# Optimization experiments

Hardware: AMD Instinct MI355X
Metric: run time of the kernel (lower is better)

## Reference

```python
import jax, jax.numpy as jnp
import numpy as np

D_MODEL = 1024
N_HEADS = 16
D_K = D_MODEL // N_HEADS


def setup_inputs() -> dict:
    key = jax.random.key(0)
    k1, k2, k3 = jax.random.split(key, 3)
    x = jax.random.normal(k1, (2, 2048, D_MODEL), dtype=jnp.float32)
    # torch Linear(d, 3d).weight has shape [3d, d]; y = x @ W.T
    W_qkv = jax.random.normal(k2, (3 * D_MODEL, D_MODEL), dtype=jnp.float32) * (1.0 / np.sqrt(D_MODEL))
    W_out = jax.random.normal(k3, (D_MODEL, D_MODEL), dtype=jnp.float32) * (1.0 / np.sqrt(D_MODEL))
    return {"x": x, "W_qkv": W_qkv, "W_out": W_out}


def reference(x, W_qkv, W_out):
    batch, seq_len, d_model = x.shape
    qkv = jnp.einsum('bsd,ed->bse', x, W_qkv)  # [b, s, 3*d_model]
    qkv = qkv.reshape(batch, seq_len, 3, N_HEADS, D_K)
    qkv = jnp.transpose(qkv, (2, 0, 3, 1, 4))  # [3, b, h, s, dk]
    Q, K, V = qkv[0], qkv[1], qkv[2]
    scale = 1.0 / jnp.sqrt(jnp.asarray(D_K, dtype=x.dtype))
    scores = jnp.einsum('bhqd,bhkd->bhqk', Q, K) * scale  # [b, h, s, s]
    causal = jnp.tril(jnp.ones((seq_len, seq_len), dtype=bool))
    scores = jnp.where(causal, scores, jnp.asarray(-jnp.inf, dtype=scores.dtype))
    attn = jax.nn.softmax(scores, axis=-1)
    out = jnp.einsum('bhqk,bhkd->bhqd', attn, V)  # [b, h, s, dk]
    out = jnp.transpose(out, (0, 2, 1, 3)).reshape(batch, seq_len, d_model)
    return jnp.einsum('bsd,ed->bse', out, W_out)
```

## Files before the change

### kernel.cpp

```cpp
#include <hip/hip_runtime.h>
#include <stdint.h>

#define DMODEL 1024
#define NHEADS 16
#define DKH 64
#define BATCH 2
#define SEQ 2048
#define MTOT (BATCH*SEQ)

typedef __bf16 bf16x8 __attribute__((ext_vector_type(8)));
typedef __bf16 bf16x4 __attribute__((ext_vector_type(4)));
typedef float  f32x4  __attribute__((ext_vector_type(4)));

__device__ __forceinline__ f32x4 mfma16(bf16x8 a, bf16x8 b, f32x4 c){
  return __builtin_amdgcn_mfma_f32_16x16x32_bf16(a, b, c, 0, 0, 0);
}

__device__ __forceinline__ void gload_lds16(const void* g, void* l){
  __builtin_amdgcn_global_load_lds(
      (const __attribute__((address_space(1))) uint32_t*)(uintptr_t)g,
      (__attribute__((address_space(3))) uint32_t*)(uint32_t)(uintptr_t)l,
      16, 0, 0);
}

__device__ __forceinline__ unsigned short f2bf(float f){
  unsigned u = __builtin_bit_cast(unsigned, f);
  u += 0x7fff + ((u >> 16) & 1);
  return (unsigned short)(u >> 16);
}

__global__ void cvt_kernel(const float* __restrict__ in, unsigned short* __restrict__ out, int n4){
  const float4*  in4  = (const float4*)in;
  ushort4*       out4 = (ushort4*)out;
  int i = blockIdx.x * blockDim.x + threadIdx.x;
  int stride = gridDim.x * blockDim.x;
  for (; i < n4; i += stride){
    float4 v = in4[i];
    ushort4 o;
    o.x = f2bf(v.x); o.y = f2bf(v.y); o.z = f2bf(v.z); o.w = f2bf(v.w);
    out4[i] = o;
  }
}

template<int EPI>
__global__ __launch_bounds__(256)
void gemm_bt(const __bf16* __restrict__ Ag, const __bf16* __restrict__ Bg,
             int M, int N, int K,
             __bf16* __restrict__ Qo, __bf16* __restrict__ Ko, __bf16* __restrict__ Vt,
             float* __restrict__ Co){
  __shared__ __align__(16) __bf16 As[128*32];
  __shared__ __align__(16) __bf16 Bs[128*32];
  const int tid  = threadIdx.x;
  const int wave = tid >> 6, lane = tid & 63;
  const int wr = wave >> 1, wc = wave & 1;
  const int lr = lane & 15, lg = lane >> 4;
  const int m0 = blockIdx.y * 128, n0 = blockIdx.x * 128;

  f32x4 acc[4][4] = {};

  const int srow = lane >> 2;
  const int scol = (lane & 3) * 8;
  const __bf16* gA = Ag + (size_t)(m0 + wave*32 + srow) * K + scol;
  const __bf16* gB = Bg + (size_t)(n0 + wave*32 + srow) * K + scol;
  __bf16* lA = &As[(wave*32) * 32];
  __bf16* lB = &Bs[(wave*32) * 32];

  for (int k0 = 0; k0 < K; k0 += 32){
    __syncthreads();
    gload_lds16(gA + k0,                lA);
    gload_lds16(gA + k0 + (size_t)16*K, lA + 16*32);
    gload_lds16(gB + k0,                lB);
    gload_lds16(gB + k0 + (size_t)16*K, lB + 16*32);
    __syncthreads();

    bf16x8 af[4], bfv[4];
#pragma unroll
    for (int i = 0; i < 4; i++)
      af[i] = *(const bf16x8*)&As[(wr*64 + i*16 + lr)*32 + lg*8];
#pragma unroll
    for (int j = 0; j < 4; j++)
      bfv[j] = *(const bf16x8*)&Bs[(wc*64 + j*16 + lr)*32 + lg*8];
#pragma unroll
    for (int i = 0; i < 4; i++)
#pragma unroll
      for (int j = 0; j < 4; j++)
        acc[i][j] = mfma16(af[i], bfv[j], acc[i][j]);
  }

  if (EPI == 0){
    const int three = n0 >> 10;
#pragma unroll
    for (int i = 0; i < 4; i++){
#pragma unroll
      for (int j = 0; j < 4; j++){
#pragma unroll
        for (int r = 0; r < 4; r++){
          int m = m0 + wr*64 + i*16 + lg*4 + r;
          int n = n0 + wc*64 + j*16 + lr;
          int b = m >> 11, s = m & 2047;
          int h = (n >> 6) & 15, dk = n & 63;
          __bf16 val = (__bf16)acc[i][j][r];
          if (three == 0)      Qo[(((size_t)(b*NHEADS + h))*SEQ + s)*DKH + dk] = val;
          else if (three == 1) Ko[(((size_t)(b*NHEADS + h))*SEQ + s)*DKH + dk] = val;
          else                 Vt[(((size_t)(b*NHEADS + h))*DKH + dk)*SEQ + s] = val;
        }
      }
    }
  } else {
#pragma unroll
    for (int i = 0; i < 4; i++)
#pragma unroll
      for (int j = 0; j < 4; j++)
#pragma unroll
        for (int r = 0; r < 4; r++){
          int m = m0 + wr*64 + i*16 + lg*4 + r;
          int n = n0 + wc*64 + j*16 + lr;
          Co[(size_t)m * N + n] = acc[i][j][r];
        }
  }
}

__global__ __launch_bounds__(128)
void attn_kernel(const __bf16* __restrict__ Q, const __bf16* __restrict__ K,
                 const __bf16* __restrict__ Vt, __bf16* __restrict__ Aout){
  const int id   = blockIdx.x;
  const int xcd  = id & 7;
  const int slot = id >> 3;
  const int bh   = (xcd << 2) | (slot >> 5);
  const int j    = slot & 31;
  const int wave = threadIdx.x >> 6, lane = threadIdx.x & 63;
  const int lr = lane & 15, lg = lane >> 4;
  const int swz = (lr & 7) << 4;

  const __bf16* Qh = Q + (size_t)bh*SEQ*DKH;
  const char* Kc = (const char*)(K  + (size_t)bh*SEQ*DKH);
  const char* Vc = (const char*)(Vt + (size_t)bh*DKH*SEQ);

  __shared__ __align__(16) char lds[2][16384];

  const int row8 = lane >> 3;
  const int cG   = ((lane & 7) << 4) ^ (row8 << 4);

  const int b = bh >> 4, h = bh & 15;
  const float k2 = 0.125f * 1.44269504088896340736f;

  for (int ph = 0; ph < 2; ph++){
    const int tb  = ph ? (63 - j) : j;
    const int qw  = tb*32 + wave*16;
    const int nkv = (tb >> 1) + 1;

    bf16x8 qf0 = *(const bf16x8*)(Qh + (size_t)(qw + lr)*DKH + lg*8);
    bf16x8 qf1 = *(const bf16x8*)(Qh + (size_t)(qw + lr)*DKH + 32 + lg*8);

    f32x4 o[4] = {};
    float mrun = -1e30f, lrun = 0.f;

#pragma unroll
    for (int i = 0; i < 4; i++){
      const int srow = wave*32 + i*8 + row8;
      gload_lds16(Kc + (size_t)srow*128 + cG,  &lds[0][wave*4096 + i*1024]);
      gload_lds16(Vc + (size_t)srow*4096 + cG, &lds[0][8192 + wave*4096 + i*1024]);
    }
    __syncthreads();

    for (int kb = 0; kb < nkv; kb++){
      const int kv0 = kb*64;
      if (kb + 1 < nkv){
        const int nv0 = kv0 + 64;
#pragma unroll
        for (int i = 0; i < 4; i++){
          const int srow = wave*32 + i*8 + row8;
          gload_lds16(Kc + (size_t)(nv0 + srow)*128 + cG,
                      &lds[(kb+1)&1][wave*4096 + i*1024]);
          gload_lds16(Vc + (size_t)srow*4096 + (size_t)nv0*2 + cG,
                      &lds[(kb+1)&1][8192 + wave*4096 + i*1024]);
        }
      }
      const char* Ks = lds[kb&1];
      const char* Vs = lds[kb&1] + 8192;

      f32x4 sf[4];
      __builtin_amdgcn_s_setprio(1);
#pragma unroll
      for (int t = 0; t < 4; t++){
        const int row = t*16 + lr;
        bf16x8 kf0 = *(const bf16x8*)(Ks + row*128 + ((lg*16) ^ swz));
        bf16x8 kf1 = *(const bf16x8*)(Ks + row*128 + ((64 + lg*16) ^ swz));
        f32x4 c = {};
        c = mfma16(kf0, qf0, c);
        c = mfma16(kf1, qf1, c);
        sf[t] = c;
      }
      __builtin_amdgcn_s_setprio(0);
      if (kv0 + 63 > qw){
        const int q = qw + lr;
#pragma unroll
        for (int t = 0; t < 4; t++)
#pragma unroll
          for (int r = 0; r < 4; r++){
            int kv = kv0 + t*16 + lg*4 + r;
            sf[t][r] = (kv <= q) ? sf[t][r]*k2 : -1e30f;
          }
      } else {
#pragma unroll
        for (int t = 0; t < 4; t++)
#pragma unroll
          for (int r = 0; r < 4; r++)
            sf[t][r] *= k2;
      }
      float mx = sf[0][0];
#pragma unroll
      for (int t = 0; t < 4; t++)
#pragma unroll
        for (int r = 0; r < 4; r++) mx = fmaxf(mx, sf[t][r]);
      mx = fmaxf(mx, __shfl_xor(mx, 16));
      mx = fmaxf(mx, __shfl_xor(mx, 32));

      float mn = fmaxf(mrun, mx);
      float alpha = __builtin_amdgcn_exp2f(mrun - mn);
      mrun = mn;
      lrun *= alpha;

      float p[16];
#pragma unroll
      for (int t = 0; t < 4; t++)
#pragma unroll
        for (int r = 0; r < 4; r++){
          float v = __builtin_amdgcn_exp2f(sf[t][r] - mn);
          p[t*4 + r] = v;
          lrun += v;
        }

      float av[4];
#pragma unroll
      for (int r = 0; r < 4; r++) av[r] = __shfl(alpha, lg*4 + r);
#pragma unroll
      for (int n = 0; n < 4; n++)
#pragma unroll
        for (int r = 0; r < 4; r++) o[n][r] *= av[r];

      bf16x8 pa0, pa1;
#pragma unroll
      for (int i = 0; i < 8; i++){ pa0[i] = (__bf16)p[i]; pa1[i] = (__bf16)p[8 + i]; }
      __builtin_amdgcn_s_setprio(1);
#pragma unroll
      for (int n = 0; n < 4; n++){
        const int row = n*16 + lr;
        bf16x4 vlo0 = *(const bf16x4*)(Vs + row*128 + ((lg*8) ^ swz));
        bf16x4 vhi0 = *(const bf16x4*)(Vs + row*128 + ((32 + lg*8) ^ swz));
        bf16x4 vlo1 = *(const bf16x4*)(Vs + row*128 + ((64 + lg*8) ^ swz));
        bf16x4 vhi1 = *(const bf16x4*)(Vs + row*128 + ((96 + lg*8) ^ swz));
        bf16x8 vf0 = __builtin_shufflevector(vlo0, vhi0, 0,1,2,3,4,5,6,7);
        bf16x8 vf1 = __builtin_shufflevector(vlo1, vhi1, 0,1,2,3,4,5,6,7);
        o[n] = mfma16(pa0, vf0, o[n]);
        o[n] = mfma16(pa1, vf1, o[n]);
      }
      __builtin_amdgcn_s_setprio(0);
      __syncthreads();
    }

    lrun += __shfl_xor(lrun, 16);
    lrun += __shfl_xor(lrun, 32);
    float inv = 1.0f / lrun;
#pragma unroll
    for (int r = 0; r < 4; r++){
      float invr = __shfl(inv, lg*4 + r);
      __bf16* dst = Aout + ((size_t)b*SEQ + qw + lg*4 + r)*DMODEL + h*DKH;
#pragma unroll
      for (int n = 0; n < 4; n++)
        dst[n*16 + lr] = (__bf16)(o[n][r] * invr);
    }
  }
}

extern "C" void kernel_launch(void* const* d_in, const int* in_sizes, int n_in,
                              void* d_out, int out_size, void* d_ws, size_t ws_size,
                              hipStream_t stream){
  const float* x    = (const float*)d_in[0];
  const float* wqkv = (const float*)d_in[1];
  const float* wout = (const float*)d_in[2];
  float* out = (float*)d_out;
  char* ws = (char*)d_ws;

  __bf16* xb  = (__bf16*)(ws);
  __bf16* Ab  = (__bf16*)(ws);
  __bf16* wqb = (__bf16*)(ws + 8388608);
  __bf16* wob = (__bf16*)(ws + 14680064);
  __bf16* Qb  = (__bf16*)(ws + 16777216);
  __bf16* Kb  = (__bf16*)(ws + 25165824);
  __bf16* Vtb = (__bf16*)(ws + 33554432);

  cvt_kernel<<<1024, 256, 0, stream>>>(x,    (unsigned short*)xb,  (MTOT*DMODEL)/4);
  cvt_kernel<<<1024, 256, 0, stream>>>(wqkv, (unsigned short*)wqb, (3*DMODEL*DMODEL)/4);
  cvt_kernel<<<256,  256, 0, stream>>>(wout, (unsigned short*)wob, (DMODEL*DMODEL)/4);

  gemm_bt<0><<<dim3(24, 32), 256, 0, stream>>>(xb, wqb, MTOT, 3*DMODEL, DMODEL,
                                               Qb, Kb, Vtb, nullptr);
  attn_kernel<<<1024, 128, 0, stream>>>(Qb, Kb, Vtb, Ab);
  gemm_bt<1><<<dim3(8, 32), 256, 0, stream>>>(Ab, wob, MTOT, DMODEL, DMODEL,
                                              nullptr, nullptr, nullptr, out);
}
```

Baseline: 203.5 us.

## Double-buffer GEMM loads, fold softmax scale into Q, lazy rescale in attention

The GEMM now double-buffers its LDS tiles so the next K-slice loads while the current one is multiplied, removing one barrier per iteration. It is templated on tile size, and the output projection uses 128x64 tiles to launch more blocks. The softmax scale times log2(e) is folded into Q in the QKV epilogue, so attention no longer multiplies every score. Attention also skips the running-max rescale unless the new max exceeds the old by more than 8 in log2 units. That lazy rescale is exact after final normalization but allows larger intermediate exponentials, and rounding the pre-scaled Q to bf16 slightly changes numerics.

```diff
diff --git a/kernel.cpp b/kernel.cpp
--- a/kernel.cpp
+++ b/kernel.cpp
@@ -28,6 +28,8 @@
   u += 0x7fff + ((u >> 16) & 1);
   return (unsigned short)(u >> 16);
 }
+
+#define QSCALE 0.1803368801111372f
 
 __global__ void cvt_kernel(const float* __restrict__ in, unsigned short* __restrict__ out, int n4){
   const float4*  in4  = (const float4*)in;
@@ -42,79 +44,93 @@
   }
 }
 
-template<int EPI>
+template<int EPI, int BM, int BN>
 __global__ __launch_bounds__(256)
 void gemm_bt(const __bf16* __restrict__ Ag, const __bf16* __restrict__ Bg,
              int M, int N, int K,
              __bf16* __restrict__ Qo, __bf16* __restrict__ Ko, __bf16* __restrict__ Vt,
              float* __restrict__ Co){
-  __shared__ __align__(16) __bf16 As[128*32];
-  __shared__ __align__(16) __bf16 Bs[128*32];
+  constexpr int AM = BM/32;
+  constexpr int AN = BN/32;
+  constexpr int CA = BM/64;
+  constexpr int CB = BN/64;
+  __shared__ __align__(16) __bf16 As[2][BM*32];
+  __shared__ __align__(16) __bf16 Bs[2][BN*32];
   const int tid  = threadIdx.x;
   const int wave = tid >> 6, lane = tid & 63;
   const int wr = wave >> 1, wc = wave & 1;
   const int lr = lane & 15, lg = lane >> 4;
-  const int m0 = blockIdx.y * 128, n0 = blockIdx.x * 128;
-
-  f32x4 acc[4][4] = {};
+  const int m0 = blockIdx.y * BM, n0 = blockIdx.x * BN;
+
+  f32x4 acc[AM][AN] = {};
 
   const int srow = lane >> 2;
   const int scol = (lane & 3) * 8;
-  const __bf16* gA = Ag + (size_t)(m0 + wave*32 + srow) * K + scol;
-  const __bf16* gB = Bg + (size_t)(n0 + wave*32 + srow) * K + scol;
-  __bf16* lA = &As[(wave*32) * 32];
-  __bf16* lB = &Bs[(wave*32) * 32];
-
-  for (int k0 = 0; k0 < K; k0 += 32){
+  const __bf16* gA = Ag + (size_t)(m0 + wave*(BM/4) + srow) * K + scol;
+  const __bf16* gB = Bg + (size_t)(n0 + wave*(BN/4) + srow) * K + scol;
+
+  const int nk = K >> 5;
+
+#pragma unroll
+  for (int c = 0; c < CA; c++)
+    gload_lds16(gA + (size_t)(c*16)*K, &As[0][(wave*(BM/4) + c*16)*32]);
+#pragma unroll
+  for (int c = 0; c < CB; c++)
+    gload_lds16(gB + (size_t)(c*16)*K, &Bs[0][(wave*(BN/4) + c*16)*32]);
+
+  for (int t = 0; t < nk; t++){
     __syncthreads();
-    gload_lds16(gA + k0,                lA);
-    gload_lds16(gA + k0 + (size_t)16*K, lA + 16*32);
-    gload_lds16(gB + k0,                lB);
-    gload_lds16(gB + k0 + (size_t)16*K, lB + 16*32);
-    __syncthreads();
-
-    bf16x8 af[4], bfv[4];
-#pragma unroll
-    for (int i = 0; i < 4; i++)
-      af[i] = *(const bf16x8*)&As[(wr*64 + i*16 + lr)*32 + lg*8];
-#pragma unroll
-    for (int j = 0; j < 4; j++)
-      bfv[j] = *(const bf16x8*)&Bs[(wc*64 + j*16 + lr)*32 + lg*8];
-#pragma unroll
-    for (int i = 0; i < 4; i++)
-#pragma unroll
-      for (int j = 0; j < 4; j++)
+    if (t + 1 < nk){
+      const int k0 = (t+1) << 5, b = (t+1) & 1;
+#pragma unroll
+      for (int c = 0; c < CA; c++)
+        gload_lds16(gA + k0 + (size_t)(c*16)*K, &As[b][(wave*(BM/4) + c*16)*32]);
+#pragma unroll
+      for (int c = 0; c < CB; c++)
+        gload_lds16(gB + k0 + (size_t)(c*16)*K, &Bs[b][(wave*(BN/4) + c*16)*32]);
+    }
+    const int cb = t & 1;
+    bf16x8 af[AM], bfv[AN];
+#pragma unroll
+    for (int i = 0; i < AM; i++)
+      af[i] = *(const bf16x8*)&As[cb][(wr*(BM/2) + i*16 + lr)*32 + lg*8];
+#pragma unroll
+    for (int j = 0; j < AN; j++)
+      bfv[j] = *(const bf16x8*)&Bs[cb][(wc*(BN/2) + j*16 + lr)*32 + lg*8];
+#pragma unroll
+    for (int i = 0; i < AM; i++)
+#pragma unroll
+      for (int j = 0; j < AN; j++)
         acc[i][j] = mfma16(af[i], bfv[j], acc[i][j]);
   }
 
   if (EPI == 0){
     const int three = n0 >> 10;
 #pragma unroll
-    for (int i = 0; i < 4; i++){
-#pragma unroll
-      for (int j = 0; j < 4; j++){
+    for (int i = 0; i < AM; i++){
+#pragma unroll
+      for (int j = 0; j < AN; j++){
 #pragma unroll
         for (int r = 0; r < 4; r++){
-          int m = m0 + wr*64 + i*16 + lg*4 + r;
-          int n = n0 + wc*64 + j*16 + lr;
+          int m = m0 + wr*(BM/2) + i*16 + lg*4 + r;
+          int n = n0 + wc*(BN/2) + j*16 + lr;
           int b = m >> 11, s = m & 2047;
           int h = (n >> 6) & 15, dk = n & 63;
-          __bf16 val = (__bf16)acc[i][j][r];
-          if (three == 0)      Qo[(((size_t)(b*NHEADS + h))*SEQ + s)*DKH + dk] = val;
-          else if (three == 1) Ko[(((size_t)(b*NHEADS + h))*SEQ + s)*DKH + dk] = val;
-          else                 Vt[(((size_t)(b*NHEADS + h))*DKH + dk)*SEQ + s] = val;
+          if (three == 0)      Qo[(((size_t)(b*NHEADS + h))*SEQ + s)*DKH + dk] = (__bf16)(acc[i][j][r] * QSCALE);
+          else if (three == 1) Ko[(((size_t)(b*NHEADS + h))*SEQ + s)*DKH + dk] = (__bf16)acc[i][j][r];
+          else                 Vt[(((size_t)(b*NHEADS + h))*DKH + dk)*SEQ + s] = (__bf16)acc[i][j][r];
         }
       }
     }
   } else {
 #pragma unroll
-    for (int i = 0; i < 4; i++)
-#pragma unroll
-      for (int j = 0; j < 4; j++)
+    for (int i = 0; i < AM; i++)
+#pragma unroll
+      for (int j = 0; j < AN; j++)
 #pragma unroll
         for (int r = 0; r < 4; r++){
-          int m = m0 + wr*64 + i*16 + lg*4 + r;
-          int n = n0 + wc*64 + j*16 + lr;
+          int m = m0 + wr*(BM/2) + i*16 + lg*4 + r;
+          int n = n0 + wc*(BN/2) + j*16 + lr;
           Co[(size_t)m * N + n] = acc[i][j][r];
         }
   }
@@ -142,7 +158,6 @@
   const int cG   = ((lane & 7) << 4) ^ (row8 << 4);
 
   const int b = bh >> 4, h = bh & 15;
-  const float k2 = 0.125f * 1.44269504088896340736f;
 
   for (int ph = 0; ph < 2; ph++){
     const int tb  = ph ? (63 - j) : j;
@@ -199,45 +214,40 @@
 #pragma unroll
           for (int r = 0; r < 4; r++){
             int kv = kv0 + t*16 + lg*4 + r;
-            sf[t][r] = (kv <= q) ? sf[t][r]*k2 : -1e30f;
+            sf[t][r] = (kv <= q) ? sf[t][r] : -1e30f;
           }
-      } else {
-#pragma unroll
-        for (int t = 0; t < 4; t++)
-#pragma unroll
-          for (int r = 0; r < 4; r++)
-            sf[t][r] *= k2;
-      }
-      float mx = sf[0][0];
-#pragma unroll
-      for (int t = 0; t < 4; t++)
-#pragma unroll
-        for (int r = 0; r < 4; r++) mx = fmaxf(mx, sf[t][r]);
+      }
+      float mx = fmaxf(fmaxf(fmaxf(sf[0][0], sf[0][1]), fmaxf(sf[0][2], sf[0][3])),
+                       fmaxf(fmaxf(sf[1][0], sf[1][1]), fmaxf(sf[1][2], sf[1][3])));
+      float mx2 = fmaxf(fmaxf(fmaxf(sf[2][0], sf[2][1]), fmaxf(sf[2][2], sf[2][3])),
+                        fmaxf(fmaxf(sf[3][0], sf[3][1]), fmaxf(sf[3][2], sf[3][3])));
+      mx = fmaxf(mx, mx2);
       mx = fmaxf(mx, __shfl_xor(mx, 16));
       mx = fmaxf(mx, __shfl_xor(mx, 32));
 
-      float mn = fmaxf(mrun, mx);
-      float alpha = __builtin_amdgcn_exp2f(mrun - mn);
-      mrun = mn;
-      lrun *= alpha;
+      if (!__all(mx <= mrun + 8.0f)){
+        float mn = fmaxf(mrun, mx);
+        float alpha = __builtin_amdgcn_exp2f(mrun - mn);
+        mrun = mn;
+        lrun *= alpha;
+        float av[4];
+#pragma unroll
+        for (int r = 0; r < 4; r++) av[r] = __shfl(alpha, lg*4 + r);
+#pragma unroll
+        for (int n = 0; n < 4; n++)
+#pragma unroll
+          for (int r = 0; r < 4; r++) o[n][r] *= av[r];
+      }
 
       float p[16];
 #pragma unroll
       for (int t = 0; t < 4; t++)
 #pragma unroll
         for (int r = 0; r < 4; r++){
-          float v = __builtin_amdgcn_exp2f(sf[t][r] - mn);
+          float v = __builtin_amdgcn_exp2f(sf[t][r] - mrun);
           p[t*4 + r] = v;
           lrun += v;
         }
-
-      float av[4];
-#pragma unroll
-      for (int r = 0; r < 4; r++) av[r] = __shfl(alpha, lg*4 + r);
-#pragma unroll
-      for (int n = 0; n < 4; n++)
-#pragma unroll
-        for (int r = 0; r < 4; r++) o[n][r] *= av[r];
 
       bf16x8 pa0, pa1;
 #pragma unroll
@@ -294,9 +304,9 @@
   cvt_kernel<<<1024, 256, 0, stream>>>(wqkv, (unsigned short*)wqb, (3*DMODEL*DMODEL)/4);
   cvt_kernel<<<256,  256, 0, stream>>>(wout, (unsigned short*)wob, (DMODEL*DMODEL)/4);
 
-  gemm_bt<0><<<dim3(24, 32), 256, 0, stream>>>(xb, wqb, MTOT, 3*DMODEL, DMODEL,
-                                               Qb, Kb, Vtb, nullptr);
+  gemm_bt<0,128,128><<<dim3(24, 32), 256, 0, stream>>>(xb, wqb, MTOT, 3*DMODEL, DMODEL,
+                                                       Qb, Kb, Vtb, nullptr);
   attn_kernel<<<1024, 128, 0, stream>>>(Qb, Kb, Vtb, Ab);
-  gemm_bt<1><<<dim3(8, 32), 256, 0, stream>>>(Ab, wob, MTOT, DMODEL, DMODEL,
-                                              nullptr, nullptr, nullptr, out);
-}
+  gemm_bt<1,128,64><<<dim3(16, 32), 256, 0, stream>>>(Ab, wob, MTOT, DMODEL, DMODEL,
+                                                      nullptr, nullptr, nullptr, out);
+}
```

New measurement: 184.4 us. 9.4% less time.
